# Performance work log

Hardware: AMD Instinct MI355X
Metric: run time of the kernel (lower is better)

## Reference

```python
import jax, jax.numpy as jnp
import numpy as np

EPS = 1e-5
COORD_TAU, COORD_KAPPA = 1.0, 1.0
COT_TAU, COT_LAM = 0.8, 0.7
GATE_FLOOR = 0.05


def _gconv(x, w, b=None):
    # grouped 1x1 conv: x [B,C,H,W], w [g, co_per_g, ci_per_g]
    B, C, H, W = x.shape
    g, co, ci = w.shape
    y = jnp.einsum('goi,bgihw->bgohw', w, x.reshape(B, g, ci, H, W)).reshape(B, g * co, H, W)
    return y if b is None else y + b[None, :, None, None]


def _conv1x1(x, w):
    # dense 1x1 conv: w [Cout, Cin]
    return jnp.einsum('oi,bihw->bohw', w, x)


def _inorm(x, g, b):
    # InstanceNorm2d(affine=True): per (B,C) stats over spatial dims, biased var
    mu = x.mean(axis=(2, 3), keepdims=True)
    var = x.var(axis=(2, 3), keepdims=True)
    return (x - mu) * jax.lax.rsqrt(var + EPS) * g[None, :, None, None] + b[None, :, None, None]


def _axis_softmax(z, L, axis):
    # stabilized softmax along a spatial axis, mean-rescaled by L
    zz = z / COORD_TAU
    zz = zz - zz.max(axis=axis, keepdims=True)
    return jax.nn.softmax(zz, axis=axis) * L


def _forward(x, compress_w, inc_g, inc_b, coord_proj_w, coord_proj_g, coord_proj_b,
             coord_h_w, coord_h_b, coord_wc_w, coord_wc_b, coord_alpha, coord_beta,
             cot_key_w, cot_val_w, cot_att1_w, cot_attn_g, cot_attn_b, cot_att2_w,
             cot_fuse_w, fusion_w, fus_g, fus_b, gate_w, expand_w):
    xc = jax.nn.relu(_inorm(_conv1x1(x, compress_w), inc_g, inc_b))  # [B,m,H,W]
    B, C, H, W = xc.shape

    # ---- Coord2H branch (use_softmax=True path) ----
    def proj(t):
        return jax.nn.silu(_inorm(_gconv(t, coord_proj_w), coord_proj_g, coord_proj_b))

    zh = _gconv(proj(xc.mean(axis=3, keepdims=True)), coord_h_w, coord_h_b)   # [B,C,H,1]
    zw = _gconv(proj(xc.mean(axis=2, keepdims=True)), coord_wc_w, coord_wc_b)  # [B,C,1,W]
    ah = _axis_softmax(zh, H, 2)
    aw = _axis_softmax(zw, W, 3)
    w_lin = coord_alpha * ah + coord_beta * aw  # broadcasts to [B,C,H,W]
    coord_out = xc * (1.0 + COORD_KAPPA * (w_lin - 1.0))

    # ---- CoT branch ----
    k1 = _gconv(xc, cot_key_w)
    v = _gconv(xc, cot_val_w)
    y = jnp.concatenate([k1, xc], axis=1)  # [B,2C,H,W]
    att = jax.nn.relu(_inorm(_gconv(y, cot_att1_w), cot_attn_g, cot_attn_b))
    att_logits = _gconv(att, cot_att2_w)
    z = (att_logits / COT_TAU).reshape(B, C, H * W)
    sm = jax.nn.softmax(z - z.max(axis=-1, keepdims=True), axis=-1).reshape(B, C, H, W) * (H * W)
    att_mix = (1.0 - COT_LAM) * jax.nn.sigmoid(att_logits) + COT_LAM * sm
    cot_out = _conv1x1(k1 + att_mix * v, cot_fuse_w)

    # ---- fusion + gate + expand ----
    fused = jax.nn.relu(_inorm(_conv1x1(jnp.concatenate([coord_out, cot_out], axis=1), fusion_w), fus_g, fus_b))
    gate = jax.nn.sigmoid(jnp.einsum('oi,bi->bo', gate_w, fused.mean(axis=(2, 3))))[:, :, None, None]  # [B,1,1,1]
    return _conv1x1(fused * (gate * (1.0 - GATE_FLOOR) + GATE_FLOOR), expand_w)


def setup_inputs() -> dict:
    key = jax.random.key(0)
    B, DIM, H, W = 8, 512, 128, 128
    RED, G = 16, 4
    m = DIM // RED  # 32
    mg = m // G     # 8
    ks = jax.random.split(key, 23)

    def n(k, s, sc=0.05):
        return jax.random.normal(k, s, dtype=jnp.float32) * sc

    return {
        'x': jax.random.normal(ks[0], (B, DIM, H, W), dtype=jnp.float32),
        'compress_w': n(ks[1], (m, DIM)),
        'inc_g': 1.0 + n(ks[2], (m,)),
        'inc_b': n(ks[3], (m,)),
        'coord_proj_w': n(ks[4], (G, mg, mg), 0.2),
        'coord_proj_g': 1.0 + n(ks[5], (m,)),
        'coord_proj_b': n(ks[6], (m,)),
        'coord_h_w': n(ks[7], (G, mg, mg), 0.2),
        'coord_h_b': n(ks[8], (m,)),
        'coord_wc_w': n(ks[9], (G, mg, mg), 0.2),
        'coord_wc_b': n(ks[10], (m,)),
        'coord_alpha': jnp.asarray(0.5, dtype=jnp.float32),
        'coord_beta': jnp.asarray(0.5, dtype=jnp.float32),
        'cot_key_w': n(ks[11], (G, mg, mg), 0.2),
        'cot_val_w': n(ks[12], (G, mg, mg), 0.2),
        'cot_att1_w': n(ks[13], (G, mg, 2 * mg), 0.2),
        'cot_attn_g': 1.0 + n(ks[14], (m,)),
        'cot_attn_b': n(ks[15], (m,)),
        'cot_att2_w': n(ks[16], (G, mg, mg), 0.2),
        'cot_fuse_w': n(ks[17], (m, m), 0.1),
        'fusion_w': n(ks[18], (m, 2 * m), 0.1),
        'fus_g': 1.0 + n(ks[19], (m,)),
        'fus_b': n(ks[20], (m,)),
        'gate_w': n(ks[21], (1, m), 0.2),
        'expand_w': n(ks[22], (DIM, m), 0.1),
    }


def reference(x, compress_w, inc_g, inc_b, coord_proj_w, coord_proj_g, coord_proj_b,
              coord_h_w, coord_h_b, coord_wc_w, coord_wc_b, coord_alpha, coord_beta,
              cot_key_w, cot_val_w, cot_att1_w, cot_attn_g, cot_attn_b, cot_att2_w,
              cot_fuse_w, fusion_w, fus_g, fus_b, gate_w, expand_w):
    return _forward(x, compress_w, inc_g, inc_b, coord_proj_w, coord_proj_g, coord_proj_b,
                    coord_h_w, coord_h_b, coord_wc_w, coord_wc_b, coord_alpha, coord_beta,
                    cot_key_w, cot_val_w, cot_att1_w, cot_attn_g, cot_attn_b, cot_att2_w,
                    cot_fuse_w, fusion_w, fus_g, fus_b, gate_w, expand_w)
```

## Files before the change

kernel.cpp:

```cpp
#include <hip/hip_runtime.h>
#include <math.h>

#define NB 8
#define CIN 512
#define CM 32
#define MG 8
#define HH 128
#define WW 128
#define HWSZ (HH*WW)
#define EPSF 1e-5f
#define COT_ITAU 1.25f
#define LAM 0.7f
#define GFLOOR 0.05f

typedef float vf4 __attribute__((ext_vector_type(4)));

__device__ __forceinline__ float wsum(float v){
#pragma unroll
  for (int o = 32; o; o >>= 1) v += __shfl_xor(v, o, 64);
  return v;
}

__global__ void k_tw(const float* __restrict__ w, float* __restrict__ wT){
  int i = blockIdx.x*256 + threadIdx.x;
  if (i < CM*CIN){
    int c = i >> 9, k = i & (CIN-1);
    wT[k*CM + c] = w[i];
  }
}

__global__ __launch_bounds__(256) void k_compress(
    const float* __restrict__ x, const float* __restrict__ wT,
    float* __restrict__ y, float* __restrict__ s1, float* __restrict__ s2)
{
  int tid = threadIdx.x;
  int b = blockIdx.x >> 6;
  int p = ((blockIdx.x & 63) << 8) + tid;
  const float* xb = x + ((size_t)b*CIN)*HWSZ + p;
  float acc[CM];
#pragma unroll
  for (int c=0;c<CM;c++) acc[c]=0.f;
  float xv[8], xn[8];
#pragma unroll
  for (int u=0;u<8;u++) xv[u] = __builtin_nontemporal_load(&xb[(size_t)u*HWSZ]);
  for (int i=0;i<CIN;i+=8){
    if (i+8<CIN){
#pragma unroll
      for (int u=0;u<8;u++) xn[u] = __builtin_nontemporal_load(&xb[(size_t)(i+8+u)*HWSZ]);
    }
#pragma unroll
    for (int u=0;u<8;u++){
      const float* wr = wT + (i+u)*CM;
#pragma unroll
      for (int c=0;c<CM;c++) acc[c]=fmaf(wr[c],xv[u],acc[c]);
    }
#pragma unroll
    for (int u=0;u<8;u++) xv[u]=xn[u];
  }
  float* yb = y + ((size_t)b*CM)*HWSZ + p;
#pragma unroll
  for (int c=0;c<CM;c++) yb[(size_t)c*HWSZ] = acc[c];
  float ms=0.f, mq=0.f;
#pragma unroll
  for (int c=0;c<CM;c++){
    float s = wsum(acc[c]);
    float q = wsum(acc[c]*acc[c]);
    if ((tid&63)==c){ ms=s; mq=q; }
  }
  int lane = tid & 63;
  if (lane < CM){
    atomicAdd(&s1[b*CM+lane], ms);
    atomicAdd(&s2[b*CM+lane], mq);
  }
}

__global__ void k_finalize(const float* __restrict__ s1, const float* __restrict__ s2,
    const float* __restrict__ g, const float* __restrict__ bi,
    float* __restrict__ A, float* __restrict__ Bo, float cnt)
{
  int i = threadIdx.x;
  if (i < NB*CM){
    int c = i & (CM-1);
    float mu = s1[i]/cnt;
    float var = s2[i]/cnt - mu*mu;
    float a = rsqrtf(var+EPSF)*g[c];
    A[i]=a; Bo[i]=bi[c]-mu*a;
  }
}

__global__ __launch_bounds__(256) void k_pools(const float* __restrict__ y,
    const float* __restrict__ A, const float* __restrict__ Bo,
    float* __restrict__ hpool, float* __restrict__ wpool)
{
  __shared__ float colacc[WW];
  int bc = blockIdx.x;
  int rg = blockIdx.y;
  int tid = threadIdx.x;
  float a=A[bc], bb=Bo[bc];
  if (tid<WW) colacc[tid]=0.f;
  __syncthreads();
  const float4* yp = (const float4*)(y + (size_t)bc*HWSZ + (size_t)rg*32*WW);
  int col4 = tid & 31;
  float c0=0.f,c1=0.f,c2=0.f,c3=0.f;
#pragma unroll
  for (int it=0; it<4; ++it){
    int row = (tid>>5) + it*8;
    float4 t = yp[row*32 + col4];
    float v0=fmaxf(0.f,fmaf(t.x,a,bb)), v1=fmaxf(0.f,fmaf(t.y,a,bb));
    float v2=fmaxf(0.f,fmaf(t.z,a,bb)), v3=fmaxf(0.f,fmaf(t.w,a,bb));
    c0+=v0; c1+=v1; c2+=v2; c3+=v3;
    float rs = v0+v1+v2+v3;
#pragma unroll
    for (int o=16;o;o>>=1) rs += __shfl_xor(rs,o,64);
    if ((tid&31)==0) hpool[bc*HH + rg*32 + row] = rs*(1.0f/WW);
  }
  int cb = col4*4;
  atomicAdd(&colacc[cb+0],c0); atomicAdd(&colacc[cb+1],c1);
  atomicAdd(&colacc[cb+2],c2); atomicAdd(&colacc[cb+3],c3);
  __syncthreads();
  if (tid<WW) atomicAdd(&wpool[bc*WW+tid], colacc[tid]*(1.0f/HH));
}

__global__ __launch_bounds__(256) void k_cot1(
  const float* __restrict__ y, const float* __restrict__ A, const float* __restrict__ Bo,
  const float* __restrict__ kw, const float* __restrict__ a1w,
  float* __restrict__ ao, float* __restrict__ s1, float* __restrict__ s2)
{
  int tid=threadIdx.x;
  int b = blockIdx.x >> 6;
  int p = ((blockIdx.x&63)<<8)+tid;
  size_t base = ((size_t)b*CM)*HWSZ + p;
  float xc[CM], k1[CM], at[CM];
#pragma unroll
  for (int c=0;c<CM;c++)
    xc[c] = fmaxf(0.f, fmaf(y[base+(size_t)c*HWSZ], A[b*CM+c], Bo[b*CM+c]));
#pragma unroll
  for (int gI=0;gI<4;gI++)
#pragma unroll
    for (int o=0;o<MG;o++){
      float sk=0.f;
#pragma unroll
      for (int i=0;i<MG;i++) sk = fmaf(kw[gI*64+o*8+i], xc[gI*MG+i], sk);
      k1[gI*MG+o]=sk;
    }
#pragma unroll
  for (int gI=0;gI<4;gI++)
#pragma unroll
    for (int o=0;o<MG;o++){
      float s=0.f;
#pragma unroll
      for (int i=0;i<16;i++){
        float inp = (gI<2) ? k1[gI*16+i] : xc[(gI-2)*16+i];
        s = fmaf(a1w[gI*128+o*16+i], inp, s);
      }
      at[gI*MG+o]=s;
    }
#pragma unroll
  for (int c=0;c<CM;c++) ao[base+(size_t)c*HWSZ]=at[c];
  float ms=0.f,mq=0.f;
#pragma unroll
  for (int c=0;c<CM;c++){
    float s=wsum(at[c]); float q=wsum(at[c]*at[c]);
    if ((tid&63)==c){ms=s;mq=q;}
  }
  int lane=tid&63;
  if (lane<CM){ atomicAdd(&s1[b*CM+lane],ms); atomicAdd(&s2[b*CM+lane],mq); }
}

__global__ __launch_bounds__(256) void k_cot2(
  const float* __restrict__ ao, const float* __restrict__ A, const float* __restrict__ Bo,
  const float* __restrict__ a2w,
  const float* __restrict__ hpool, const float* __restrict__ wpool,
  const float* __restrict__ pjw, const float* __restrict__ pjg, const float* __restrict__ pjb,
  const float* __restrict__ chw, const float* __restrict__ chb,
  const float* __restrict__ cww, const float* __restrict__ cwb,
  float* __restrict__ es, float* __restrict__ ah, float* __restrict__ aw)
{
  __shared__ float T[CM][HH+1];
  __shared__ float sa[CM], sb[CM], smx[CM], ssc[CM];
  int tid=threadIdx.x;
  int blk=blockIdx.x;
  int b = blk >> 6;
  int p = ((blk&63)<<8)+tid;
  size_t base = ((size_t)b*CM)*HWSZ + p;
  float att[CM], l[CM];
#pragma unroll
  for (int c=0;c<CM;c++)
    att[c] = fmaxf(0.f, fmaf(ao[base+(size_t)c*HWSZ], A[b*CM+c], Bo[b*CM+c]));
#pragma unroll
  for (int gI=0;gI<4;gI++)
#pragma unroll
    for (int o=0;o<MG;o++){
      float s=0.f;
#pragma unroll
      for (int i=0;i<MG;i++) s = fmaf(a2w[gI*64+o*8+i], att[gI*8+i], s);
      l[gI*MG+o]=s;
    }
  float ms=0.f;
#pragma unroll
  for (int c=0;c<CM;c++){
    float s = wsum(__expf(l[c]*COT_ITAU));
    if ((tid&63)==c) ms=s;
  }
  int lane=tid&63;
  if (lane<CM) atomicAdd(&es[b*CM+lane], ms);

  if (blk < 2*NB){
    int bb = blk>>1, path = blk&1;
    const float* pool = path ? wpool : hpool;
    const float* w2   = path ? cww : chw;
    const float* b2   = path ? cwb : chb;
    float* outp       = path ? aw  : ah;
    float z[CM];
    if (tid<HH){
      float in[CM];
#pragma unroll
      for (int c=0;c<CM;c++) in[c] = pool[(bb*CM+c)*HH + tid];
#pragma unroll
      for (int gI=0;gI<4;gI++)
#pragma unroll
        for (int o=0;o<MG;o++){
          float s=0.f;
#pragma unroll
          for (int i=0;i<MG;i++) s = fmaf(pjw[gI*64+o*8+i], in[gI*8+i], s);
          T[gI*8+o][tid] = s;
        }
    }
    __syncthreads();
    if (tid < CM){
      float s=0.f, q=0.f;
      for (int k=0;k<HH;k++){ float t=T[tid][k]; s+=t; q+=t*t; }
      float mu = s*(1.0f/HH);
      float var = q*(1.0f/HH) - mu*mu;
      float a = rsqrtf(var+EPSF)*pjg[tid];
      sa[tid]=a; sb[tid]=pjb[tid]-mu*a;
    }
    __syncthreads();
    if (tid<HH){
      float sil[CM];
#pragma unroll
      for (int c=0;c<CM;c++){
        float val = fmaf(T[c][tid], sa[c], sb[c]);
        sil[c] = val/(1.f+__expf(-val));
      }
#pragma unroll
      for (int gI=0;gI<4;gI++)
#pragma unroll
        for (int o=0;o<MG;o++){
          float s=b2[gI*8+o];
#pragma unroll
          for (int i=0;i<MG;i++) s = fmaf(w2[gI*64+o*8+i], sil[gI*8+i], s);
          z[gI*8+o]=s;
        }
    }
    __syncthreads();
    if (tid<HH){
#pragma unroll
      for (int c=0;c<CM;c++) T[c][tid]=z[c];
    }
    __syncthreads();
    if (tid < CM){
      float mx=-1e30f;
      for (int k=0;k<HH;k++) mx = fmaxf(mx, T[tid][k]);
      float s=0.f;
      for (int k=0;k<HH;k++) s += __expf(T[tid][k]-mx);
      smx[tid]=mx; ssc[tid]=(float)HH/s;
    }
    __syncthreads();
    if (tid<HH){
#pragma unroll
      for (int c=0;c<CM;c++)
        outp[(bb*CM+c)*HH + tid] = __expf(T[c][tid]-smx[c])*ssc[c];
    }
  }
}

__global__ __launch_bounds__(256) void k_mix_fuse(
  const float* __restrict__ y, const float* __restrict__ A, const float* __restrict__ Bo,
  const float* __restrict__ ao, const float* __restrict__ attA, const float* __restrict__ attB,
  const float* __restrict__ kw, const float* __restrict__ vw, const float* __restrict__ a2w,
  const float* __restrict__ ah, const float* __restrict__ awp, const float* __restrict__ es,
  const float* __restrict__ alpha, const float* __restrict__ beta,
  const float* __restrict__ fw, const float* __restrict__ fuw,
  float* __restrict__ fpo, float* __restrict__ s1, float* __restrict__ s2)
{
  int tid=threadIdx.x;
  int b = blockIdx.x>>6;
  int p = ((blockIdx.x&63)<<8)+tid;
  int h = p >> 7, w = p & (WW-1);
  size_t base = ((size_t)b*CM)*HWSZ + p;
  float al=alpha[0], be=beta[0];
  float xc[CM], att[CM], l[CM], t[CM];
#pragma unroll
  for (int c=0;c<CM;c++)
    xc[c] = fmaxf(0.f, fmaf(y[base+(size_t)c*HWSZ], A[b*CM+c], Bo[b*CM+c]));
#pragma unroll
  for (int c=0;c<CM;c++)
    att[c] = fmaxf(0.f, fmaf(ao[base+(size_t)c*HWSZ], attA[b*CM+c], attB[b*CM+c]));
#pragma unroll
  for (int gI=0;gI<4;gI++)
#pragma unroll
    for (int o=0;o<MG;o++){
      float s=0.f;
#pragma unroll
      for (int i=0;i<MG;i++) s = fmaf(a2w[gI*64+o*8+i], att[gI*8+i], s);
      l[gI*MG+o]=s;
    }
#pragma unroll
  for (int gI=0;gI<4;gI++)
#pragma unroll
    for (int o=0;o<MG;o++){
      float sk=0.f, sv=0.f;
#pragma unroll
      for (int i=0;i<MG;i++){
        float xv = xc[gI*MG+i];
        sk = fmaf(kw[gI*64+o*8+i], xv, sk);
        sv = fmaf(vw[gI*64+o*8+i], xv, sv);
      }
      int c = gI*MG+o;
      float lgv = l[c];
      float sm = __expf(lgv*COT_ITAU) * (16384.f/es[b*CM+c]);
      float sg = 1.f/(1.f+__expf(-lgv));
      float mix = (1.f-LAM)*sg + LAM*sm;
      t[c] = fmaf(mix, sv, sk);
    }
  float co[CM];
#pragma unroll
  for (int c=0;c<CM;c++){
    float wl = al*ah[(b*CM+c)*HH + h] + be*awp[(b*CM+c)*WW + w];
    co[c] = xc[c] * wl;
  }
  float cot[CM];
#pragma unroll
  for (int o=0;o<CM;o++){
    float s=0.f;
#pragma unroll
    for (int i=0;i<CM;i++) s = fmaf(fw[o*CM+i], t[i], s);
    cot[o]=s;
  }
  float ms=0.f, mq=0.f;
#pragma unroll
  for (int o=0;o<CM;o++){
    float s=0.f;
#pragma unroll
    for (int i=0;i<CM;i++) s = fmaf(fuw[o*64+i], co[i], s);
#pragma unroll
    for (int i=0;i<CM;i++) s = fmaf(fuw[o*64+32+i], cot[i], s);
    fpo[base+(size_t)o*HWSZ]=s;
    float ss = wsum(s); float qq = wsum(s*s);
    if ((tid&63)==o){ ms=ss; mq=qq; }
  }
  int lane=tid&63;
  if (lane<CM){ atomicAdd(&s1[b*CM+lane],ms); atomicAdd(&s2[b*CM+lane],mq); }
}

__global__ __launch_bounds__(256) void k_gstat(const float4* __restrict__ fp,
  const float* __restrict__ A, const float* __restrict__ Bo, float* __restrict__ gsum)
{
  int idx = blockIdx.x*256+threadIdx.x;
  int bc = idx >> 12;
  float a=A[bc], bb=Bo[bc];
  float4 tv = fp[idx];
  float s = fmaxf(0.f,fmaf(tv.x,a,bb))+fmaxf(0.f,fmaf(tv.y,a,bb))
          + fmaxf(0.f,fmaf(tv.z,a,bb))+fmaxf(0.f,fmaf(tv.w,a,bb));
  s = wsum(s);
  if ((threadIdx.x&63)==0) atomicAdd(&gsum[bc], s);
}

__global__ void k_gate(const float* __restrict__ gsum, const float* __restrict__ gw,
                       float* __restrict__ scale){
  int b = threadIdx.x;
  if (b < NB){
    float s=0.f;
    for (int c=0;c<CM;c++) s += gw[c]*gsum[b*CM+c];
    s *= (1.0f/HWSZ);
    float gt = 1.f/(1.f+__expf(-s));
    scale[b] = gt*(1.f-GFLOOR)+GFLOOR;
  }
}

__global__ __launch_bounds__(256) void k_expand(const float4* __restrict__ fp4,
  const float* __restrict__ A, const float* __restrict__ Bo,
  const float* __restrict__ ew, const float* __restrict__ scale, vf4* __restrict__ out4)
{
  int tid = threadIdx.x;
  int b = blockIdx.x >> 4;
  int tile = blockIdx.x & 15;
  int p4 = tile*256 + tid;
  int og = blockIdx.y * 64;
  float sc = scale[b];
  float4 f[CM];
  const float4* fb = fp4 + ((size_t)b*CM)*(HWSZ/4) + p4;
#pragma unroll
  for (int c=0;c<CM;c++){
    float4 t = fb[(size_t)c*(HWSZ/4)];
    float a=A[b*CM+c], bb=Bo[b*CM+c];
    f[c].x = fmaxf(0.f, fmaf(t.x,a,bb))*sc;
    f[c].y = fmaxf(0.f, fmaf(t.y,a,bb))*sc;
    f[c].z = fmaxf(0.f, fmaf(t.z,a,bb))*sc;
    f[c].w = fmaxf(0.f, fmaf(t.w,a,bb))*sc;
  }
  vf4* ob = out4 + ((size_t)b*CIN + og)*(HWSZ/4) + p4;
  for (int j=0;j<64;j++){
    const float* wr = ew + (og+j)*CM;
    vf4 acc = (vf4)(0.f);
#pragma unroll
    for (int c=0;c<CM;c++){
      float wv = wr[c];
      acc.x = fmaf(wv, f[c].x, acc.x);
      acc.y = fmaf(wv, f[c].y, acc.y);
      acc.z = fmaf(wv, f[c].z, acc.z);
      acc.w = fmaf(wv, f[c].w, acc.w);
    }
    __builtin_nontemporal_store(acc, &ob[(size_t)j*(HWSZ/4)]);
  }
}

extern "C" void kernel_launch(void* const* d_in, const int* in_sizes, int n_in,
                              void* d_out, int out_size, void* d_ws, size_t ws_size,
                              hipStream_t stream)
{
  const float* x    = (const float*)d_in[0];
  const float* cw   = (const float*)d_in[1];
  const float* incg = (const float*)d_in[2];
  const float* incb = (const float*)d_in[3];
  const float* pjw  = (const float*)d_in[4];
  const float* pjg  = (const float*)d_in[5];
  const float* pjb  = (const float*)d_in[6];
  const float* chw  = (const float*)d_in[7];
  const float* chb  = (const float*)d_in[8];
  const float* cww  = (const float*)d_in[9];
  const float* cwb  = (const float*)d_in[10];
  const float* alpha= (const float*)d_in[11];
  const float* beta = (const float*)d_in[12];
  const float* kw   = (const float*)d_in[13];
  const float* vw   = (const float*)d_in[14];
  const float* a1w  = (const float*)d_in[15];
  const float* ag   = (const float*)d_in[16];
  const float* ab   = (const float*)d_in[17];
  const float* a2w  = (const float*)d_in[18];
  const float* fw   = (const float*)d_in[19];
  const float* fuw  = (const float*)d_in[20];
  const float* fg   = (const float*)d_in[21];
  const float* fb   = (const float*)d_in[22];
  const float* gw   = (const float*)d_in[23];
  const float* ew   = (const float*)d_in[24];
  float* out = (float*)d_out;

  float* ws = (float*)d_ws;
  const size_t BIG = (size_t)NB*CM*HWSZ;
  float* y    = ws;
  float* P    = ws +   BIG;
  float* F    = ws + 2*BIG;
  float* sm   = ws + 3*BIG;
  float* acc   = sm;  sm += 2048;
  float* statS = acc,      *statQ = acc+256;
  float* attS  = acc+512,  *attQ  = acc+768;
  float* esum  = acc+1024;
  float* fusS  = acc+1280, *fusQ  = acc+1536;
  float* gsum  = acc+1792;
  float* wpool = sm;  sm += NB*CM*WW;
  float* wT    = sm;  sm += CM*CIN;
  float* hpool = sm;  sm += NB*CM*HH;
  float* ahB   = sm;  sm += NB*CM*HH;
  float* awB   = sm;  sm += NB*CM*WW;
  float* normA = sm; sm+=256; float* normB = sm; sm+=256;
  float* attA  = sm; sm+=256; float* attB  = sm; sm+=256;
  float* fusA  = sm; sm+=256; float* fusB  = sm; sm+=256;
  float* scale = sm; sm+=64;

  hipMemsetAsync(acc, 0, (2048 + NB*CM*WW)*sizeof(float), stream);
  k_tw<<<64,256,0,stream>>>(cw, wT);
  k_compress<<<512,256,0,stream>>>(x, wT, y, statS, statQ);
  k_finalize<<<1,256,0,stream>>>(statS,statQ,incg,incb,normA,normB,(float)HWSZ);
  k_pools<<<dim3(NB*CM,4),256,0,stream>>>(y,normA,normB,hpool,wpool);
  k_cot1<<<512,256,0,stream>>>(y,normA,normB,kw,a1w,P,attS,attQ);
  k_finalize<<<1,256,0,stream>>>(attS,attQ,ag,ab,attA,attB,(float)HWSZ);
  k_cot2<<<512,256,0,stream>>>(P,attA,attB,a2w,hpool,wpool,pjw,pjg,pjb,chw,chb,cww,cwb,esum,ahB,awB);
  k_mix_fuse<<<512,256,0,stream>>>(y,normA,normB,P,attA,attB,kw,vw,a2w,ahB,awB,esum,alpha,beta,fw,fuw,F,fusS,fusQ);
  k_finalize<<<1,256,0,stream>>>(fusS,fusQ,fg,fb,fusA,fusB,(float)HWSZ);
  k_gstat<<<4096,256,0,stream>>>((const float4*)F, fusA,fusB,gsum);
  k_gate<<<1,64,0,stream>>>(gsum,gw,scale);
  k_expand<<<dim3(128,8),256,0,stream>>>((const float4*)F,fusA,fusB,ew,scale,(vf4*)out);
}
```

Before: 356.0 us.

## Recompute CoT attention in consumers, fold norm finalize into kernels, split-K compress

The intermediate attention tensor P is no longer written to and read from global memory. Each consumer kernel recomputes k1 and the att1 conv from y instead, trading extra ALU work for less memory traffic. The separate finalize and gate kernels are removed, and each consumer derives the InstanceNorm scale and shift from the accumulated sums, which cuts launch count. The compress kernel now splits the input channels across two half-blocks and combines them through shared memory, doubling the grid to raise occupancy over the 512-channel reduction.

```diff
diff --git a/kernel.cpp b/kernel.cpp
--- a/kernel.cpp
+++ b/kernel.cpp
@@ -33,70 +33,75 @@
     const float* __restrict__ x, const float* __restrict__ wT,
     float* __restrict__ y, float* __restrict__ s1, float* __restrict__ s2)
 {
+  __shared__ float comb[CM][128];
   int tid = threadIdx.x;
-  int b = blockIdx.x >> 6;
-  int p = ((blockIdx.x & 63) << 8) + tid;
-  const float* xb = x + ((size_t)b*CIN)*HWSZ + p;
+  int lp  = tid & 127;
+  int kh  = tid >> 7;
+  int pos = blockIdx.x*128 + lp;
+  int b   = pos >> 14;
+  int pp  = pos & (HWSZ-1);
+  const float* xb = x + ((size_t)b*CIN + kh*256)*HWSZ + pp;
+  const float* wh = wT + kh*256*CM;
   float acc[CM];
 #pragma unroll
   for (int c=0;c<CM;c++) acc[c]=0.f;
   float xv[8], xn[8];
 #pragma unroll
   for (int u=0;u<8;u++) xv[u] = __builtin_nontemporal_load(&xb[(size_t)u*HWSZ]);
-  for (int i=0;i<CIN;i+=8){
-    if (i+8<CIN){
+  for (int i=0;i<256;i+=8){
+    if (i+8<256){
 #pragma unroll
       for (int u=0;u<8;u++) xn[u] = __builtin_nontemporal_load(&xb[(size_t)(i+8+u)*HWSZ]);
     }
 #pragma unroll
     for (int u=0;u<8;u++){
-      const float* wr = wT + (i+u)*CM;
+      const float* wr = wh + (i+u)*CM;
 #pragma unroll
       for (int c=0;c<CM;c++) acc[c]=fmaf(wr[c],xv[u],acc[c]);
     }
 #pragma unroll
     for (int u=0;u<8;u++) xv[u]=xn[u];
   }
-  float* yb = y + ((size_t)b*CM)*HWSZ + p;
-#pragma unroll
-  for (int c=0;c<CM;c++) yb[(size_t)c*HWSZ] = acc[c];
-  float ms=0.f, mq=0.f;
-#pragma unroll
-  for (int c=0;c<CM;c++){
-    float s = wsum(acc[c]);
-    float q = wsum(acc[c]*acc[c]);
-    if ((tid&63)==c){ ms=s; mq=q; }
-  }
-  int lane = tid & 63;
-  if (lane < CM){
-    atomicAdd(&s1[b*CM+lane], ms);
-    atomicAdd(&s2[b*CM+lane], mq);
-  }
-}
-
-__global__ void k_finalize(const float* __restrict__ s1, const float* __restrict__ s2,
-    const float* __restrict__ g, const float* __restrict__ bi,
-    float* __restrict__ A, float* __restrict__ Bo, float cnt)
-{
-  int i = threadIdx.x;
-  if (i < NB*CM){
-    int c = i & (CM-1);
-    float mu = s1[i]/cnt;
-    float var = s2[i]/cnt - mu*mu;
-    float a = rsqrtf(var+EPSF)*g[c];
-    A[i]=a; Bo[i]=bi[c]-mu*a;
+  if (kh){
+#pragma unroll
+    for (int c=0;c<CM;c++) comb[c][lp]=acc[c];
+  }
+  __syncthreads();
+  if (!kh){
+#pragma unroll
+    for (int c=0;c<CM;c++) acc[c]+=comb[c][lp];
+    float* yb = y + ((size_t)b*CM)*HWSZ + pp;
+#pragma unroll
+    for (int c=0;c<CM;c++) yb[(size_t)c*HWSZ]=acc[c];
+    float ms=0.f, mq=0.f;
+#pragma unroll
+    for (int c=0;c<CM;c++){
+      float s = wsum(acc[c]);
+      float q = wsum(acc[c]*acc[c]);
+      if ((tid&63)==c){ ms=s; mq=q; }
+    }
+    int lane = tid & 63;
+    if (lane < CM){
+      atomicAdd(&s1[b*CM+lane], ms);
+      atomicAdd(&s2[b*CM+lane], mq);
+    }
   }
 }
 
 __global__ __launch_bounds__(256) void k_pools(const float* __restrict__ y,
-    const float* __restrict__ A, const float* __restrict__ Bo,
+    const float* __restrict__ s1, const float* __restrict__ s2,
+    const float* __restrict__ incg, const float* __restrict__ incb,
     float* __restrict__ hpool, float* __restrict__ wpool)
 {
   __shared__ float colacc[WW];
   int bc = blockIdx.x;
   int rg = blockIdx.y;
   int tid = threadIdx.x;
-  float a=A[bc], bb=Bo[bc];
+  int c = bc & (CM-1);
+  float mu  = s1[bc]*(1.f/HWSZ);
+  float var = fmaf(-mu,mu, s2[bc]*(1.f/HWSZ));
+  float a   = rsqrtf(var+EPSF)*incg[c];
+  float bb  = incb[c]-mu*a;
   if (tid<WW) colacc[tid]=0.f;
   __syncthreads();
   const float4* yp = (const float4*)(y + (size_t)bc*HWSZ + (size_t)rg*32*WW);
@@ -121,19 +126,29 @@
   if (tid<WW) atomicAdd(&wpool[bc*WW+tid], colacc[tid]*(1.0f/HH));
 }
 
-__global__ __launch_bounds__(256) void k_cot1(
-  const float* __restrict__ y, const float* __restrict__ A, const float* __restrict__ Bo,
+__global__ __launch_bounds__(256) void k_attstat(
+  const float* __restrict__ y,
+  const float* __restrict__ s1i, const float* __restrict__ s2i,
+  const float* __restrict__ incg, const float* __restrict__ incb,
   const float* __restrict__ kw, const float* __restrict__ a1w,
-  float* __restrict__ ao, float* __restrict__ s1, float* __restrict__ s2)
-{
+  float* __restrict__ s1, float* __restrict__ s2)
+{
+  __shared__ float nA[CM], nB[CM];
   int tid=threadIdx.x;
   int b = blockIdx.x >> 6;
   int p = ((blockIdx.x&63)<<8)+tid;
+  if (tid<CM){
+    float mu  = s1i[b*CM+tid]*(1.f/HWSZ);
+    float var = fmaf(-mu,mu, s2i[b*CM+tid]*(1.f/HWSZ));
+    float a   = rsqrtf(var+EPSF)*incg[tid];
+    nA[tid]=a; nB[tid]=incb[tid]-mu*a;
+  }
+  __syncthreads();
   size_t base = ((size_t)b*CM)*HWSZ + p;
   float xc[CM], k1[CM], at[CM];
 #pragma unroll
   for (int c=0;c<CM;c++)
-    xc[c] = fmaxf(0.f, fmaf(y[base+(size_t)c*HWSZ], A[b*CM+c], Bo[b*CM+c]));
+    xc[c] = fmaxf(0.f, fmaf(y[base+(size_t)c*HWSZ], nA[c], nB[c]));
 #pragma unroll
   for (int gI=0;gI<4;gI++)
 #pragma unroll
@@ -155,8 +170,6 @@
       }
       at[gI*MG+o]=s;
     }
-#pragma unroll
-  for (int c=0;c<CM;c++) ao[base+(size_t)c*HWSZ]=at[c];
   float ms=0.f,mq=0.f;
 #pragma unroll
   for (int c=0;c<CM;c++){
@@ -168,8 +181,12 @@
 }
 
 __global__ __launch_bounds__(256) void k_cot2(
-  const float* __restrict__ ao, const float* __restrict__ A, const float* __restrict__ Bo,
-  const float* __restrict__ a2w,
+  const float* __restrict__ y,
+  const float* __restrict__ s1i, const float* __restrict__ s2i,
+  const float* __restrict__ incg, const float* __restrict__ incb,
+  const float* __restrict__ s1a, const float* __restrict__ s2a,
+  const float* __restrict__ ag, const float* __restrict__ ab,
+  const float* __restrict__ kw, const float* __restrict__ a1w, const float* __restrict__ a2w,
   const float* __restrict__ hpool, const float* __restrict__ wpool,
   const float* __restrict__ pjw, const float* __restrict__ pjg, const float* __restrict__ pjb,
   const float* __restrict__ chw, const float* __restrict__ chb,
@@ -178,22 +195,58 @@
 {
   __shared__ float T[CM][HH+1];
   __shared__ float sa[CM], sb[CM], smx[CM], ssc[CM];
+  __shared__ float nA[CM], nB[CM], tA[CM], tB[CM];
   int tid=threadIdx.x;
   int blk=blockIdx.x;
   int b = blk >> 6;
   int p = ((blk&63)<<8)+tid;
+  if (tid<CM){
+    float mu  = s1i[b*CM+tid]*(1.f/HWSZ);
+    float var = fmaf(-mu,mu, s2i[b*CM+tid]*(1.f/HWSZ));
+    float a   = rsqrtf(var+EPSF)*incg[tid];
+    nA[tid]=a; nB[tid]=incb[tid]-mu*a;
+    float mu2  = s1a[b*CM+tid]*(1.f/HWSZ);
+    float var2 = fmaf(-mu2,mu2, s2a[b*CM+tid]*(1.f/HWSZ));
+    float a2   = rsqrtf(var2+EPSF)*ag[tid];
+    tA[tid]=a2; tB[tid]=ab[tid]-mu2*a2;
+  }
+  __syncthreads();
   size_t base = ((size_t)b*CM)*HWSZ + p;
-  float att[CM], l[CM];
+  float xc[CM], k1[CM], at[CM], l[CM];
 #pragma unroll
   for (int c=0;c<CM;c++)
-    att[c] = fmaxf(0.f, fmaf(ao[base+(size_t)c*HWSZ], A[b*CM+c], Bo[b*CM+c]));
+    xc[c] = fmaxf(0.f, fmaf(y[base+(size_t)c*HWSZ], nA[c], nB[c]));
+#pragma unroll
+  for (int gI=0;gI<4;gI++)
+#pragma unroll
+    for (int o=0;o<MG;o++){
+      float sk=0.f;
+#pragma unroll
+      for (int i=0;i<MG;i++) sk = fmaf(kw[gI*64+o*8+i], xc[gI*MG+i], sk);
+      k1[gI*MG+o]=sk;
+    }
 #pragma unroll
   for (int gI=0;gI<4;gI++)
 #pragma unroll
     for (int o=0;o<MG;o++){
       float s=0.f;
 #pragma unroll
-      for (int i=0;i<MG;i++) s = fmaf(a2w[gI*64+o*8+i], att[gI*8+i], s);
+      for (int i=0;i<16;i++){
+        float inp = (gI<2) ? k1[gI*16+i] : xc[(gI-2)*16+i];
+        s = fmaf(a1w[gI*128+o*16+i], inp, s);
+      }
+      at[gI*MG+o]=s;
+    }
+#pragma unroll
+  for (int c=0;c<CM;c++)
+    at[c] = fmaxf(0.f, fmaf(at[c], tA[c], tB[c]));
+#pragma unroll
+  for (int gI=0;gI<4;gI++)
+#pragma unroll
+    for (int o=0;o<MG;o++){
+      float s=0.f;
+#pragma unroll
+      for (int i=0;i<MG;i++) s = fmaf(a2w[gI*64+o*8+i], at[gI*8+i], s);
       l[gI*MG+o]=s;
     }
   float ms=0.f;
@@ -276,53 +329,86 @@
 }
 
 __global__ __launch_bounds__(256) void k_mix_fuse(
-  const float* __restrict__ y, const float* __restrict__ A, const float* __restrict__ Bo,
-  const float* __restrict__ ao, const float* __restrict__ attA, const float* __restrict__ attB,
-  const float* __restrict__ kw, const float* __restrict__ vw, const float* __restrict__ a2w,
+  const float* __restrict__ y,
+  const float* __restrict__ s1i, const float* __restrict__ s2i,
+  const float* __restrict__ incg, const float* __restrict__ incb,
+  const float* __restrict__ s1a, const float* __restrict__ s2a,
+  const float* __restrict__ ag, const float* __restrict__ ab,
+  const float* __restrict__ kw, const float* __restrict__ vw,
+  const float* __restrict__ a1w, const float* __restrict__ a2w,
   const float* __restrict__ ah, const float* __restrict__ awp, const float* __restrict__ es,
   const float* __restrict__ alpha, const float* __restrict__ beta,
   const float* __restrict__ fw, const float* __restrict__ fuw,
   float* __restrict__ fpo, float* __restrict__ s1, float* __restrict__ s2)
 {
+  __shared__ float nA[CM], nB[CM], tA[CM], tB[CM];
   int tid=threadIdx.x;
   int b = blockIdx.x>>6;
   int p = ((blockIdx.x&63)<<8)+tid;
   int h = p >> 7, w = p & (WW-1);
+  if (tid<CM){
+    float mu  = s1i[b*CM+tid]*(1.f/HWSZ);
+    float var = fmaf(-mu,mu, s2i[b*CM+tid]*(1.f/HWSZ));
+    float a   = rsqrtf(var+EPSF)*incg[tid];
+    nA[tid]=a; nB[tid]=incb[tid]-mu*a;
+    float mu2  = s1a[b*CM+tid]*(1.f/HWSZ);
+    float var2 = fmaf(-mu2,mu2, s2a[b*CM+tid]*(1.f/HWSZ));
+    float a2   = rsqrtf(var2+EPSF)*ag[tid];
+    tA[tid]=a2; tB[tid]=ab[tid]-mu2*a2;
+  }
+  __syncthreads();
   size_t base = ((size_t)b*CM)*HWSZ + p;
   float al=alpha[0], be=beta[0];
-  float xc[CM], att[CM], l[CM], t[CM];
+  float xc[CM], k1[CM], at[CM], l[CM], t[CM];
 #pragma unroll
   for (int c=0;c<CM;c++)
-    xc[c] = fmaxf(0.f, fmaf(y[base+(size_t)c*HWSZ], A[b*CM+c], Bo[b*CM+c]));
+    xc[c] = fmaxf(0.f, fmaf(y[base+(size_t)c*HWSZ], nA[c], nB[c]));
+#pragma unroll
+  for (int gI=0;gI<4;gI++)
+#pragma unroll
+    for (int o=0;o<MG;o++){
+      float sk=0.f;
+#pragma unroll
+      for (int i=0;i<MG;i++) sk = fmaf(kw[gI*64+o*8+i], xc[gI*MG+i], sk);
+      k1[gI*MG+o]=sk;
+    }
+#pragma unroll
+  for (int gI=0;gI<4;gI++)
+#pragma unroll
+    for (int o=0;o<MG;o++){
+      float s=0.f;
+#pragma unroll
+      for (int i=0;i<16;i++){
+        float inp = (gI<2) ? k1[gI*16+i] : xc[(gI-2)*16+i];
+        s = fmaf(a1w[gI*128+o*16+i], inp, s);
+      }
+      at[gI*MG+o]=s;
+    }
 #pragma unroll
   for (int c=0;c<CM;c++)
-    att[c] = fmaxf(0.f, fmaf(ao[base+(size_t)c*HWSZ], attA[b*CM+c], attB[b*CM+c]));
+    at[c] = fmaxf(0.f, fmaf(at[c], tA[c], tB[c]));
 #pragma unroll
   for (int gI=0;gI<4;gI++)
 #pragma unroll
     for (int o=0;o<MG;o++){
       float s=0.f;
 #pragma unroll
-      for (int i=0;i<MG;i++) s = fmaf(a2w[gI*64+o*8+i], att[gI*8+i], s);
+      for (int i=0;i<MG;i++) s = fmaf(a2w[gI*64+o*8+i], at[gI*8+i], s);
       l[gI*MG+o]=s;
     }
 #pragma unroll
   for (int gI=0;gI<4;gI++)
 #pragma unroll
     for (int o=0;o<MG;o++){
-      float sk=0.f, sv=0.f;
-#pragma unroll
-      for (int i=0;i<MG;i++){
-        float xv = xc[gI*MG+i];
-        sk = fmaf(kw[gI*64+o*8+i], xv, sk);
-        sv = fmaf(vw[gI*64+o*8+i], xv, sv);
-      }
+      float sv=0.f;
+#pragma unroll
+      for (int i=0;i<MG;i++) sv = fmaf(vw[gI*64+o*8+i], xc[gI*MG+i], sv);
       int c = gI*MG+o;
       float lgv = l[c];
       float sm = __expf(lgv*COT_ITAU) * (16384.f/es[b*CM+c]);
       float sg = 1.f/(1.f+__expf(-lgv));
       float mix = (1.f-LAM)*sg + LAM*sm;
-      t[c] = fmaf(mix, sv, sk);
+      t[c] = fmaf(mix, sv, k1[c]);
     }
   float co[CM];
 #pragma unroll
@@ -355,11 +441,17 @@
 }
 
 __global__ __launch_bounds__(256) void k_gstat(const float4* __restrict__ fp,
-  const float* __restrict__ A, const float* __restrict__ Bo, float* __restrict__ gsum)
+  const float* __restrict__ s1f, const float* __restrict__ s2f,
+  const float* __restrict__ fg, const float* __restrict__ fb,
+  float* __restrict__ gsum)
 {
   int idx = blockIdx.x*256+threadIdx.x;
   int bc = idx >> 12;
-  float a=A[bc], bb=Bo[bc];
+  int c = bc & (CM-1);
+  float mu  = s1f[bc]*(1.f/HWSZ);
+  float var = fmaf(-mu,mu, s2f[bc]*(1.f/HWSZ));
+  float a   = rsqrtf(var+EPSF)*fg[c];
+  float bb  = fb[c]-mu*a;
   float4 tv = fp[idx];
   float s = fmaxf(0.f,fmaf(tv.x,a,bb))+fmaxf(0.f,fmaf(tv.y,a,bb))
           + fmaxf(0.f,fmaf(tv.z,a,bb))+fmaxf(0.f,fmaf(tv.w,a,bb));
@@ -367,34 +459,37 @@
   if ((threadIdx.x&63)==0) atomicAdd(&gsum[bc], s);
 }
 
-__global__ void k_gate(const float* __restrict__ gsum, const float* __restrict__ gw,
-                       float* __restrict__ scale){
-  int b = threadIdx.x;
-  if (b < NB){
-    float s=0.f;
-    for (int c=0;c<CM;c++) s += gw[c]*gsum[b*CM+c];
-    s *= (1.0f/HWSZ);
-    float gt = 1.f/(1.f+__expf(-s));
-    scale[b] = gt*(1.f-GFLOOR)+GFLOOR;
-  }
-}
-
 __global__ __launch_bounds__(256) void k_expand(const float4* __restrict__ fp4,
-  const float* __restrict__ A, const float* __restrict__ Bo,
-  const float* __restrict__ ew, const float* __restrict__ scale, vf4* __restrict__ out4)
-{
+  const float* __restrict__ s1f, const float* __restrict__ s2f,
+  const float* __restrict__ fg, const float* __restrict__ fb,
+  const float* __restrict__ gw, const float* __restrict__ gsum,
+  const float* __restrict__ ew, vf4* __restrict__ out4)
+{
+  __shared__ float fA[CM], fB[CM];
   int tid = threadIdx.x;
   int b = blockIdx.x >> 4;
   int tile = blockIdx.x & 15;
   int p4 = tile*256 + tid;
   int og = blockIdx.y * 64;
-  float sc = scale[b];
+  if (tid<CM){
+    float mu  = s1f[b*CM+tid]*(1.f/HWSZ);
+    float var = fmaf(-mu,mu, s2f[b*CM+tid]*(1.f/HWSZ));
+    float a   = rsqrtf(var+EPSF)*fg[tid];
+    fA[tid]=a; fB[tid]=fb[tid]-mu*a;
+  }
+  float s=0.f;
+#pragma unroll
+  for (int c=0;c<CM;c++) s = fmaf(gw[c], gsum[b*CM+c], s);
+  s *= (1.0f/HWSZ);
+  float gt = 1.f/(1.f+__expf(-s));
+  float sc = gt*(1.f-GFLOOR)+GFLOOR;
+  __syncthreads();
   float4 f[CM];
-  const float4* fb = fp4 + ((size_t)b*CM)*(HWSZ/4) + p4;
+  const float4* fbp = fp4 + ((size_t)b*CM)*(HWSZ/4) + p4;
 #pragma unroll
   for (int c=0;c<CM;c++){
-    float4 t = fb[(size_t)c*(HWSZ/4)];
-    float a=A[b*CM+c], bb=Bo[b*CM+c];
+    float4 t = fbp[(size_t)c*(HWSZ/4)];
+    float a=fA[c], bb=fB[c];
     f[c].x = fmaxf(0.f, fmaf(t.x,a,bb))*sc;
     f[c].y = fmaxf(0.f, fmaf(t.y,a,bb))*sc;
     f[c].z = fmaxf(0.f, fmaf(t.z,a,bb))*sc;
@@ -450,9 +545,8 @@
   float* ws = (float*)d_ws;
   const size_t BIG = (size_t)NB*CM*HWSZ;
   float* y    = ws;
-  float* P    = ws +   BIG;
-  float* F    = ws + 2*BIG;
-  float* sm   = ws + 3*BIG;
+  float* F    = ws +   BIG;
+  float* sm   = ws + 2*BIG;
   float* acc   = sm;  sm += 2048;
   float* statS = acc,      *statQ = acc+256;
   float* attS  = acc+512,  *attQ  = acc+768;
@@ -464,22 +558,16 @@
   float* hpool = sm;  sm += NB*CM*HH;
   float* ahB   = sm;  sm += NB*CM*HH;
   float* awB   = sm;  sm += NB*CM*WW;
-  float* normA = sm; sm+=256; float* normB = sm; sm+=256;
-  float* attA  = sm; sm+=256; float* attB  = sm; sm+=256;
-  float* fusA  = sm; sm+=256; float* fusB  = sm; sm+=256;
-  float* scale = sm; sm+=64;
 
   hipMemsetAsync(acc, 0, (2048 + NB*CM*WW)*sizeof(float), stream);
   k_tw<<<64,256,0,stream>>>(cw, wT);
-  k_compress<<<512,256,0,stream>>>(x, wT, y, statS, statQ);
-  k_finalize<<<1,256,0,stream>>>(statS,statQ,incg,incb,normA,normB,(float)HWSZ);
-  k_pools<<<dim3(NB*CM,4),256,0,stream>>>(y,normA,normB,hpool,wpool);
-  k_cot1<<<512,256,0,stream>>>(y,normA,normB,kw,a1w,P,attS,attQ);
-  k_finalize<<<1,256,0,stream>>>(attS,attQ,ag,ab,attA,attB,(float)HWSZ);
-  k_cot2<<<512,256,0,stream>>>(P,attA,attB,a2w,hpool,wpool,pjw,pjg,pjb,chw,chb,cww,cwb,esum,ahB,awB);
-  k_mix_fuse<<<512,256,0,stream>>>(y,normA,normB,P,attA,attB,kw,vw,a2w,ahB,awB,esum,alpha,beta,fw,fuw,F,fusS,fusQ);
-  k_finalize<<<1,256,0,stream>>>(fusS,fusQ,fg,fb,fusA,fusB,(float)HWSZ);
-  k_gstat<<<4096,256,0,stream>>>((const float4*)F, fusA,fusB,gsum);
-  k_gate<<<1,64,0,stream>>>(gsum,gw,scale);
-  k_expand<<<dim3(128,8),256,0,stream>>>((const float4*)F,fusA,fusB,ew,scale,(vf4*)out);
-}
+  k_compress<<<1024,256,0,stream>>>(x, wT, y, statS, statQ);
+  k_pools<<<dim3(NB*CM,4),256,0,stream>>>(y,statS,statQ,incg,incb,hpool,wpool);
+  k_attstat<<<512,256,0,stream>>>(y,statS,statQ,incg,incb,kw,a1w,attS,attQ);
+  k_cot2<<<512,256,0,stream>>>(y,statS,statQ,incg,incb,attS,attQ,ag,ab,kw,a1w,a2w,
+                               hpool,wpool,pjw,pjg,pjb,chw,chb,cww,cwb,esum,ahB,awB);
+  k_mix_fuse<<<512,256,0,stream>>>(y,statS,statQ,incg,incb,attS,attQ,ag,ab,kw,vw,a1w,a2w,
+                                   ahB,awB,esum,alpha,beta,fw,fuw,F,fusS,fusQ);
+  k_gstat<<<4096,256,0,stream>>>((const float4*)F,fusS,fusQ,fg,fb,gsum);
+  k_expand<<<dim3(128,8),256,0,stream>>>((const float4*)F,fusS,fusQ,fg,fb,gw,gsum,ew,(vf4*)out);
+}
```

Measured after the change: 594.7 us. 67.1% more time.
